# Kernel optimization log

Measured on AMD Instinct MI355X. Metric: run time of the kernel, lower is better.

Reference implementation:

```python
import jax, jax.numpy as jnp
import numpy as np

N = 8192      # nodes
E = 16384     # edges
G = 512       # graphs
IN = 235      # node feature dim (input_dim)
H = 64        # hidden_dim
ED = 52       # edge feature dim


def setup_inputs() -> dict:
    key = jax.random.key(0)
    ks = jax.random.split(key, 24)
    s = lambda fan_in: 1.0 / np.sqrt(fan_in)
    inp = {}
    inp["x"] = jax.random.normal(ks[0], (N, IN), dtype=jnp.float32)
    inp["edge_index"] = jax.random.randint(ks[1], (2, E), 0, N)
    inp["edge_attr"] = jax.random.uniform(ks[2], (E, ED), dtype=jnp.float32)
    inp["batch"] = jnp.sort(jax.random.randint(ks[3], (N,), 0, G))
    # EdgeModel (nn of nnconv1): Linear(52,128) -> Linear(128, 235*64)
    inp["W1"] = jax.random.normal(ks[4], (128, ED), dtype=jnp.float32) * s(ED)
    inp["b1"] = jnp.zeros((128,), jnp.float32)
    inp["W2"] = jax.random.normal(ks[5], (IN * H, 128), dtype=jnp.float32) * s(128)
    inp["b2"] = jnp.zeros((IN * H,), jnp.float32)
    # NNConv root weight and bias
    inp["root"] = jax.random.normal(ks[6], (IN, H), dtype=jnp.float32) * s(IN)
    inp["conv_b"] = jnp.zeros((H,), jnp.float32)
    # MLP head
    inp["fw1"] = jax.random.normal(ks[7], (128, H), dtype=jnp.float32) * s(H)
    inp["fb1"] = jnp.zeros((128,), jnp.float32)
    inp["fw2"] = jax.random.normal(ks[8], (256, 128), dtype=jnp.float32) * s(128)
    inp["fb2"] = jnp.zeros((256,), jnp.float32)
    inp["fw3"] = jax.random.normal(ks[9], (128, 256), dtype=jnp.float32) * s(256)
    inp["fb3"] = jnp.zeros((128,), jnp.float32)
    inp["fw4"] = jax.random.normal(ks[10], (1, 128), dtype=jnp.float32) * s(128)
    inp["fb4"] = jnp.zeros((1,), jnp.float32)
    return inp


def reference(x, edge_index, edge_attr, batch, W1, b1, W2, b2, root, conv_b,
              fw1, fb1, fw2, fb2, fw3, fb3, fw4, fb4):
    src, dst = edge_index[0], edge_index[1]
    # edge MLP -> per-edge weight matrices [E, IN, H]
    h = edge_attr @ W1.T + b1
    w = (h @ W2.T + b2).reshape(E, IN, H)
    # gather source node feats, per-edge matmul, scatter-add to destinations
    msg = jnp.einsum('ei,eih->eh', x[src], w)          # [E, H]
    agg = jax.ops.segment_sum(msg, dst, num_segments=N)  # [N, H]
    out = jax.nn.relu(agg + x @ root + conv_b)           # NNConv + ReLU
    # global mean pool per graph
    summ = jax.ops.segment_sum(out, batch, num_segments=G)
    cnt = jax.ops.segment_sum(jnp.ones((N, 1), out.dtype), batch, num_segments=G)
    pooled = summ / jnp.maximum(cnt, 1.0)                # [G, H]
    # dense MLP head
    y = jax.nn.relu(pooled @ fw1.T + fb1)
    y = jax.nn.relu(y @ fw2.T + fb2)
    y = jax.nn.relu(y @ fw3.T + fb3)
    return y @ fw4.T + fb4                               # [G, 1]
```

## Files before the change

### kernel.cpp

```cpp
#include <hip/hip_runtime.h>
#include <hip/hip_bf16.h>
#include <stdint.h>

#define N_NODES 8192
#define N_EDGES 16384
#define N_GRAPHS 512
#define IN_DIM 235
#define H_DIM 64
#define ED_DIM 52
#define HID1 128
#define KP 256
#define NB 3328
#define NBE 3456
#define NBP 3584

typedef __bf16 bf16x8 __attribute__((ext_vector_type(8)));
typedef float f32x4 __attribute__((ext_vector_type(4)));

static __device__ inline unsigned short f2bf(float f) {
    union { float f; unsigned u; } v; v.f = f;
    unsigned r = v.u + 0x7FFFu + ((v.u >> 16) & 1u);
    return (unsigned short)(r >> 16);
}

__global__ __launch_bounds__(256) void k_build_bt(const float* __restrict__ W1,
                                                  const float* __restrict__ W2,
                                                  unsigned short* __restrict__ Bt) {
    __shared__ float w1s[ED_DIM * 132];
    __shared__ float w2s[16 * 132];
    const int i = blockIdx.x;
    const int by = blockIdx.y;
    const int t = threadIdx.x;
    for (int j = t; j < ED_DIM * HID1; j += 256) {
        const int k = j / ED_DIM, d = j - k * ED_DIM;
        w1s[d * 132 + k] = W1[j];
    }
    const float* w2src = W2 + ((size_t)i * 64 + by * 16) * HID1;
    for (int j = t; j < 16 * HID1; j += 256) w2s[(j >> 7) * 132 + (j & 127)] = w2src[j];
    __syncthreads();
    const int hh = t & 15, dq = t >> 4;
    const float4* w2v = (const float4*)&w2s[hh * 132];
    #pragma unroll
    for (int m = 0; m < 4; ++m) {
        const int d = dq + m * 16;
        if (d >= ED_DIM) break;
        const float4* w1v = (const float4*)&w1s[d * 132];
        float acc = 0.f;
        #pragma unroll
        for (int k4 = 0; k4 < HID1 / 4; ++k4) {
            const float4 a = w1v[k4], b = w2v[k4];
            acc += a.x * b.x + a.y * b.y + a.z * b.z + a.w * b.w;
        }
        const int p = (by * 16 + hh) * ED_DIM + d;
        Bt[(size_t)p * KP + i] = f2bf(acc);
    }
}

__global__ __launch_bounds__(256) void k_build_ext(const float* __restrict__ root,
                                                   const float* __restrict__ W2,
                                                   const float* __restrict__ b1,
                                                   const float* __restrict__ b2,
                                                   unsigned short* __restrict__ Bt) {
    const int j = blockIdx.x;
    const int i = threadIdx.x;
    if (i >= IN_DIM) return;
    float v;
    if (j < 64) {
        v = root[i * H_DIM + j];
    } else {
        const int jj = i * H_DIM + (j - 64);
        float acc = b2[jj];
        const float* w = W2 + (size_t)jj * HID1;
        #pragma unroll 8
        for (int k = 0; k < HID1; ++k) acc += w[k] * b1[k];
        v = acc;
    }
    Bt[(size_t)(NB + j) * KP + i] = f2bf(v);
}

__global__ __launch_bounds__(256) void k_build_a(const float* __restrict__ x,
                                                 unsigned short* __restrict__ A) {
    const int j = blockIdx.x * 256 + threadIdx.x;
    const int n = j >> 8, i = j & 255;
    A[j] = (i < IN_DIM) ? f2bf(x[n * IN_DIM + i]) : (unsigned short)0;
}

__global__ __launch_bounds__(512, 2) void k_gemm(const unsigned short* __restrict__ A,
                                                 const unsigned short* __restrict__ Bt,
                                                 unsigned short* __restrict__ P,
                                                 float* __restrict__ agg,
                                                 float* __restrict__ xb2,
                                                 const float* __restrict__ conv_b) {
    __shared__ unsigned short As[2 * 256 * 32];
    __shared__ unsigned short Bs[2 * 256 * 32];
    const int t = threadIdx.x;
    const int lin = blockIdx.x;
    const int xcd = lin & 7, bi = lin >> 3;
    const int mt = (bi / 14) * 8 + xcd;
    const int nt = bi % 14;
    const int m0 = mt * 256, n0 = nt * 256;
    const int wid = t >> 6, lane = t & 63;
    const int wm = wid & 1;
    const int wn = wid >> 1;
    const int q = lane >> 4, r16 = lane & 15;

    f32x4 acc[8][4] = {};

    auto stage = [&](int k0, int buf) {
        #pragma unroll
        for (int r = 0; r < 2; ++r) {
            const int idx = r * 512 + t;
            const int row = idx >> 2;
            const int lgrp = ((idx & 3) ^ ((row >> 1) & 3)) * 8;
            const unsigned short* ga = &A[(size_t)(m0 + row) * KP + k0 + lgrp];
            const unsigned short* gb = &Bt[(size_t)(n0 + row) * KP + k0 + lgrp];
            char* la = (char*)As + buf * 16384 + r * 8192 + wid * 1024;
            char* lb = (char*)Bs + buf * 16384 + r * 8192 + wid * 1024;
            __builtin_amdgcn_global_load_lds(
                (const __attribute__((address_space(1))) unsigned int*)ga,
                (__attribute__((address_space(3))) unsigned int*)la, 16, 0, 0);
            __builtin_amdgcn_global_load_lds(
                (const __attribute__((address_space(1))) unsigned int*)gb,
                (__attribute__((address_space(3))) unsigned int*)lb, 16, 0, 0);
        }
    };

    stage(0, 0);
    const int pcq = (q ^ ((r16 >> 1) & 3)) * 8;
    #pragma unroll
    for (int it = 0; it < 8; ++it) {
        __syncthreads();
        if (it < 7) stage((it + 1) * 32, (it + 1) & 1);
        const int bo = (it & 1) * 8192;
        bf16x8 af[8], bfr[4];
        #pragma unroll
        for (int mi = 0; mi < 8; ++mi)
            af[mi] = *(const bf16x8*)(&As[bo + (wm * 128 + mi * 16 + r16) * 32 + pcq]);
        #pragma unroll
        for (int ni = 0; ni < 4; ++ni)
            bfr[ni] = *(const bf16x8*)(&Bs[bo + (wn * 64 + ni * 16 + r16) * 32 + pcq]);
        #pragma unroll
        for (int mi = 0; mi < 8; ++mi)
            #pragma unroll
            for (int ni = 0; ni < 4; ++ni)
                acc[mi][ni] = __builtin_amdgcn_mfma_f32_16x16x32_bf16(
                    bfr[ni], af[mi], acc[mi][ni], 0, 0, 0);
    }

    if (n0 < NB) {
        #pragma unroll
        for (int mi = 0; mi < 8; ++mi)
            #pragma unroll
            for (int ni = 0; ni < 4; ++ni) {
                const int row = m0 + wm * 128 + mi * 16 + r16;
                const int col = n0 + wn * 64 + ni * 16 + q * 4;
                union { unsigned short us[4]; uint2 u2; } pk;
                #pragma unroll
                for (int rr = 0; rr < 4; ++rr) pk.us[rr] = f2bf(acc[mi][ni][rr]);
                *(uint2*)(&P[(size_t)row * NB + col]) = pk.u2;
            }
    } else if (wn < 2) {
        #pragma unroll
        for (int mi = 0; mi < 8; ++mi)
            #pragma unroll
            for (int ni = 0; ni < 4; ++ni) {
                const int row = m0 + wm * 128 + mi * 16 + r16;
                const int cl = ni * 16 + q * 4;
                if (wn == 0) {
                    const float4 cb = *(const float4*)&conv_b[cl];
                    float4 v;
                    v.x = acc[mi][ni][0] + cb.x; v.y = acc[mi][ni][1] + cb.y;
                    v.z = acc[mi][ni][2] + cb.z; v.w = acc[mi][ni][3] + cb.w;
                    *(float4*)(&agg[row * H_DIM + cl]) = v;
                } else {
                    float4 v;
                    v.x = acc[mi][ni][0]; v.y = acc[mi][ni][1];
                    v.z = acc[mi][ni][2]; v.w = acc[mi][ni][3];
                    *(float4*)(&xb2[row * H_DIM + cl]) = v;
                }
            }
    }
}

__global__ __launch_bounds__(256) void k_edge(const int* __restrict__ ei,
                                              const float* __restrict__ ea,
                                              const unsigned short* __restrict__ P,
                                              const float* __restrict__ xb2,
                                              float* __restrict__ agg) {
    const int e = (blockIdx.x * 256 + threadIdx.x) >> 6;
    const int h = threadIdx.x & 63;
    if (e >= N_EDGES) return;
    const int s = ei[e], dst = ei[N_EDGES + e];
    const uint2* Pr = (const uint2*)(P + (size_t)s * NB + h * ED_DIM);
    const float4* ev = (const float4*)(ea + (size_t)e * ED_DIM);

    uint2 pv[13];
    #pragma unroll
    for (int j = 0; j < 13; ++j) pv[j] = Pr[j];
    float4 eav[13];
    #pragma unroll
    for (int j = 0; j < 13; ++j) eav[j] = ev[j];

    float acc = xb2[s * H_DIM + h];
    #pragma unroll
    for (int j = 0; j < 13; ++j) {
        union { unsigned u; float f; } a0, a1, b0, b1;
        a0.u = pv[j].x << 16; a1.u = pv[j].x & 0xffff0000u;
        b0.u = pv[j].y << 16; b1.u = pv[j].y & 0xffff0000u;
        acc += eav[j].x * a0.f + eav[j].y * a1.f
             + eav[j].z * b0.f + eav[j].w * b1.f;
    }
    atomicAdd(&agg[dst * H_DIM + h], acc);
}

__global__ __launch_bounds__(256) void k_pool(const float* __restrict__ agg,
                                              const int* __restrict__ batch,
                                              float* __restrict__ psum,
                                              float* __restrict__ pcnt) {
    const int n = (blockIdx.x * 256 + threadIdx.x) >> 6;
    const int h = threadIdx.x & 63;
    if (n >= N_NODES) return;
    const float v = fmaxf(agg[n * H_DIM + h], 0.f);
    const int g = batch[n];
    atomicAdd(&psum[g * H_DIM + h], v);
    if (h == 0) atomicAdd(&pcnt[g], 1.0f);
}

__global__ __launch_bounds__(256) void k_head(const float* __restrict__ psum,
                                              const float* __restrict__ pcnt,
                                              const float* __restrict__ fw1, const float* __restrict__ fb1,
                                              const float* __restrict__ fw2, const float* __restrict__ fb2,
                                              const float* __restrict__ fw3, const float* __restrict__ fb3,
                                              const float* __restrict__ fw4, const float* __restrict__ fb4,
                                              float* __restrict__ out) {
    __shared__ float sp[64], s1[128], s2[256], s3[128];
    const int g = blockIdx.x, t = threadIdx.x;
    if (t < 64) sp[t] = psum[g * 64 + t] / fmaxf(pcnt[g], 1.0f);
    __syncthreads();
    if (t < 128) {
        float a = fb1[t];
        const float* w = fw1 + t * 64;
        #pragma unroll 8
        for (int k = 0; k < 64; ++k) a += sp[k] * w[k];
        s1[t] = fmaxf(a, 0.f);
    }
    __syncthreads();
    {
        float a = fb2[t];
        const float* w = fw2 + t * 128;
        #pragma unroll 8
        for (int k = 0; k < 128; ++k) a += s1[k] * w[k];
        s2[t] = fmaxf(a, 0.f);
    }
    __syncthreads();
    if (t < 128) {
        float a = fb3[t];
        const float* w = fw3 + t * 256;
        #pragma unroll 8
        for (int k = 0; k < 256; ++k) a += s2[k] * w[k];
        s3[t] = fmaxf(a, 0.f);
    }
    __syncthreads();
    if (t < 64) {
        float p = s3[t] * fw4[t] + s3[t + 64] * fw4[t + 64];
        #pragma unroll
        for (int off = 32; off > 0; off >>= 1) p += __shfl_down(p, off);
        if (t == 0) out[g] = p + fb4[0];
    }
}

extern "C" void kernel_launch(void* const* d_in, const int* in_sizes, int n_in,
                              void* d_out, int out_size, void* d_ws, size_t ws_size,
                              hipStream_t stream) {
    const float* x      = (const float*)d_in[0];
    const int*   ei     = (const int*)d_in[1];
    const float* ea     = (const float*)d_in[2];
    const int*   batch  = (const int*)d_in[3];
    const float* W1     = (const float*)d_in[4];
    const float* b1     = (const float*)d_in[5];
    const float* W2     = (const float*)d_in[6];
    const float* b2     = (const float*)d_in[7];
    const float* root   = (const float*)d_in[8];
    const float* conv_b = (const float*)d_in[9];
    const float* fw1 = (const float*)d_in[10]; const float* fb1 = (const float*)d_in[11];
    const float* fw2 = (const float*)d_in[12]; const float* fb2 = (const float*)d_in[13];
    const float* fw3 = (const float*)d_in[14]; const float* fb3 = (const float*)d_in[15];
    const float* fw4 = (const float*)d_in[16]; const float* fb4 = (const float*)d_in[17];
    float* out = (float*)d_out;

    char* ws = (char*)d_ws;
    unsigned short* A   = (unsigned short*)(ws);
    unsigned short* Bt  = (unsigned short*)(ws + 4194304);
    unsigned short* P   = (unsigned short*)(ws + 6029312);
    float* agg  = (float*)(ws + 60555264);
    float* xb2  = (float*)(ws + 62652416);
    float* psum = (float*)(ws + 64749568);
    float* pcnt = (float*)(ws + 64880640);

    hipMemsetAsync(Bt, 0, (size_t)NBP * KP * sizeof(unsigned short), stream);
    hipMemsetAsync(psum, 0, (size_t)(N_GRAPHS * H_DIM + N_GRAPHS) * sizeof(float), stream);

    k_build_bt<<<dim3(IN_DIM, 4), dim3(256), 0, stream>>>(W1, W2, Bt);
    k_build_ext<<<dim3(128), dim3(256), 0, stream>>>(root, W2, b1, b2, Bt);
    k_build_a<<<dim3(N_NODES), dim3(256), 0, stream>>>(x, A);
    k_gemm<<<dim3(448), dim3(512), 0, stream>>>(A, Bt, P, agg, xb2, conv_b);
    k_edge<<<dim3(N_EDGES / 4), dim3(256), 0, stream>>>(ei, ea, P, xb2, agg);
    k_pool<<<dim3(N_NODES / 4), dim3(256), 0, stream>>>(agg, batch, psum, pcnt);
    k_head<<<dim3(N_GRAPHS), dim3(256), 0, stream>>>(psum, pcnt, fw1, fb1, fw2, fb2, fw3, fb3, fw4, fb4, out);
}
```

Measured before the change: 208.1 us.

## Fuse prep kernels, replace Bt memset with targeted zeroing, fuse pool into head

The three weight and input preparation kernels are merged into one launch. The full Bt memset is replaced by blocks that zero only the padding regions. The atomic-based pooling kernel and its memset are removed: each head block binary-searches the sorted batch array for its node range and reduces that range in shared memory before running the MLP. This cuts four launches and two memsets and removes the pooling atomics. The cost is some uneven block work in the fused prep kernel and a reliance on batch being sorted.

```diff
diff --git a/kernel.cpp b/kernel.cpp
--- a/kernel.cpp
+++ b/kernel.cpp
@@ -11,8 +11,12 @@
 #define HID1 128
 #define KP 256
 #define NB 3328
-#define NBE 3456
 #define NBP 3584
+
+#define BT_BLOCKS 940
+#define EXT_BLOCKS 128
+#define ZERO_BLOCKS 16
+#define PREP_GRID (BT_BLOCKS + EXT_BLOCKS + ZERO_BLOCKS + N_NODES)
 
 typedef __bf16 bf16x8 __attribute__((ext_vector_type(8)));
 typedef float f32x4 __attribute__((ext_vector_type(4)));
@@ -23,66 +27,83 @@
     return (unsigned short)(r >> 16);
 }
 
-__global__ __launch_bounds__(256) void k_build_bt(const float* __restrict__ W1,
-                                                  const float* __restrict__ W2,
-                                                  unsigned short* __restrict__ Bt) {
+__global__ __launch_bounds__(256) void k_prep(const float* __restrict__ x,
+                                              const float* __restrict__ W1,
+                                              const float* __restrict__ W2,
+                                              const float* __restrict__ b1,
+                                              const float* __restrict__ b2,
+                                              const float* __restrict__ root,
+                                              unsigned short* __restrict__ A,
+                                              unsigned short* __restrict__ Bt) {
     __shared__ float w1s[ED_DIM * 132];
     __shared__ float w2s[16 * 132];
-    const int i = blockIdx.x;
-    const int by = blockIdx.y;
+    const int bx = blockIdx.x;
     const int t = threadIdx.x;
-    for (int j = t; j < ED_DIM * HID1; j += 256) {
-        const int k = j / ED_DIM, d = j - k * ED_DIM;
-        w1s[d * 132 + k] = W1[j];
-    }
-    const float* w2src = W2 + ((size_t)i * 64 + by * 16) * HID1;
-    for (int j = t; j < 16 * HID1; j += 256) w2s[(j >> 7) * 132 + (j & 127)] = w2src[j];
-    __syncthreads();
-    const int hh = t & 15, dq = t >> 4;
-    const float4* w2v = (const float4*)&w2s[hh * 132];
-    #pragma unroll
-    for (int m = 0; m < 4; ++m) {
-        const int d = dq + m * 16;
-        if (d >= ED_DIM) break;
-        const float4* w1v = (const float4*)&w1s[d * 132];
-        float acc = 0.f;
-        #pragma unroll
-        for (int k4 = 0; k4 < HID1 / 4; ++k4) {
-            const float4 a = w1v[k4], b = w2v[k4];
-            acc += a.x * b.x + a.y * b.y + a.z * b.z + a.w * b.w;
-        }
-        const int p = (by * 16 + hh) * ED_DIM + d;
-        Bt[(size_t)p * KP + i] = f2bf(acc);
-    }
-}
-
-__global__ __launch_bounds__(256) void k_build_ext(const float* __restrict__ root,
-                                                   const float* __restrict__ W2,
-                                                   const float* __restrict__ b1,
-                                                   const float* __restrict__ b2,
-                                                   unsigned short* __restrict__ Bt) {
-    const int j = blockIdx.x;
-    const int i = threadIdx.x;
-    if (i >= IN_DIM) return;
-    float v;
-    if (j < 64) {
-        v = root[i * H_DIM + j];
+
+    if (bx < BT_BLOCKS) {
+        const int i = bx >> 2;
+        const int by = bx & 3;
+        for (int j = t; j < ED_DIM * HID1; j += 256) {
+            const int k = j / ED_DIM, d = j - k * ED_DIM;
+            w1s[d * 132 + k] = W1[j];
+        }
+        const float* w2src = W2 + ((size_t)i * 64 + by * 16) * HID1;
+        for (int j = t; j < 16 * HID1; j += 256) w2s[(j >> 7) * 132 + (j & 127)] = w2src[j];
+        __syncthreads();
+        const int hh = t & 15, dq = t >> 4;
+        const float4* w2v = (const float4*)&w2s[hh * 132];
+        #pragma unroll
+        for (int m = 0; m < 4; ++m) {
+            const int d = dq + m * 16;
+            if (d >= ED_DIM) break;
+            const float4* w1v = (const float4*)&w1s[d * 132];
+            float acc = 0.f;
+            #pragma unroll
+            for (int k4 = 0; k4 < HID1 / 4; ++k4) {
+                const float4 a = w1v[k4], b = w2v[k4];
+                acc += a.x * b.x + a.y * b.y + a.z * b.z + a.w * b.w;
+            }
+            const int p = (by * 16 + hh) * ED_DIM + d;
+            Bt[(size_t)p * KP + i] = f2bf(acc);
+        }
+    } else if (bx < BT_BLOCKS + EXT_BLOCKS) {
+        const int j = bx - BT_BLOCKS;
+        const int i = t;
+        if (i < IN_DIM) {
+            float v;
+            if (j < 64) {
+                v = root[i * H_DIM + j];
+            } else {
+                const int jj = i * H_DIM + (j - 64);
+                float acc = b2[jj];
+                const float* w = W2 + (size_t)jj * HID1;
+                #pragma unroll 8
+                for (int k = 0; k < HID1; ++k) acc += w[k] * b1[k];
+                v = acc;
+            }
+            Bt[(size_t)(NB + j) * KP + i] = f2bf(v);
+        }
+    } else if (bx < BT_BLOCKS + EXT_BLOCKS + ZERO_BLOCKS) {
+        const int z = bx - BT_BLOCKS - EXT_BLOCKS;
+        const int R1 = NBP * 21;
+        const int TOT = R1 + 128 * IN_DIM;
+        for (int idx = z * 256 + t; idx < TOT; idx += ZERO_BLOCKS * 256) {
+            size_t off;
+            if (idx < R1) {
+                const int r = idx / 21, c = IN_DIM + idx - (idx / 21) * 21;
+                off = (size_t)r * KP + c;
+            } else {
+                const int k = idx - R1;
+                const int r = 3456 + k / IN_DIM, c = k - (k / IN_DIM) * IN_DIM;
+                off = (size_t)r * KP + c;
+            }
+            Bt[off] = 0;
+        }
     } else {
-        const int jj = i * H_DIM + (j - 64);
-        float acc = b2[jj];
-        const float* w = W2 + (size_t)jj * HID1;
-        #pragma unroll 8
-        for (int k = 0; k < HID1; ++k) acc += w[k] * b1[k];
-        v = acc;
-    }
-    Bt[(size_t)(NB + j) * KP + i] = f2bf(v);
-}
-
-__global__ __launch_bounds__(256) void k_build_a(const float* __restrict__ x,
-                                                 unsigned short* __restrict__ A) {
-    const int j = blockIdx.x * 256 + threadIdx.x;
-    const int n = j >> 8, i = j & 255;
-    A[j] = (i < IN_DIM) ? f2bf(x[n * IN_DIM + i]) : (unsigned short)0;
+        const int j = (bx - BT_BLOCKS - EXT_BLOCKS - ZERO_BLOCKS) * 256 + t;
+        const int n = j >> 8, i = j & 255;
+        A[j] = (i < IN_DIM) ? f2bf(x[n * IN_DIM + i]) : (unsigned short)0;
+    }
 }
 
 __global__ __launch_bounds__(512, 2) void k_gemm(const unsigned short* __restrict__ A,
@@ -213,52 +234,55 @@
     atomicAdd(&agg[dst * H_DIM + h], acc);
 }
 
-__global__ __launch_bounds__(256) void k_pool(const float* __restrict__ agg,
+__global__ __launch_bounds__(256) void k_tail(const float* __restrict__ agg,
                                               const int* __restrict__ batch,
-                                              float* __restrict__ psum,
-                                              float* __restrict__ pcnt) {
-    const int n = (blockIdx.x * 256 + threadIdx.x) >> 6;
-    const int h = threadIdx.x & 63;
-    if (n >= N_NODES) return;
-    const float v = fmaxf(agg[n * H_DIM + h], 0.f);
-    const int g = batch[n];
-    atomicAdd(&psum[g * H_DIM + h], v);
-    if (h == 0) atomicAdd(&pcnt[g], 1.0f);
-}
-
-__global__ __launch_bounds__(256) void k_head(const float* __restrict__ psum,
-                                              const float* __restrict__ pcnt,
                                               const float* __restrict__ fw1, const float* __restrict__ fb1,
                                               const float* __restrict__ fw2, const float* __restrict__ fb2,
                                               const float* __restrict__ fw3, const float* __restrict__ fb3,
                                               const float* __restrict__ fw4, const float* __restrict__ fb4,
                                               float* __restrict__ out) {
+    __shared__ float red[256];
     __shared__ float sp[64], s1[128], s2[256], s3[128];
     const int g = blockIdx.x, t = threadIdx.x;
-    if (t < 64) sp[t] = psum[g * 64 + t] / fmaxf(pcnt[g], 1.0f);
-    __syncthreads();
+
+    int lo = 0, hi = N_NODES;
+    while (lo < hi) { const int mid = (lo + hi) >> 1; if (batch[mid] < g) lo = mid + 1; else hi = mid; }
+    const int start = lo;
+    hi = N_NODES;
+    while (lo < hi) { const int mid = (lo + hi) >> 1; if (batch[mid] <= g) lo = mid + 1; else hi = mid; }
+    const int end = lo;
+    const float inv = 1.0f / fmaxf((float)(end - start), 1.0f);
+
+    float a = 0.f;
+    for (int n = start + (t >> 6); n < end; n += 4)
+        a += fmaxf(agg[n * H_DIM + (t & 63)], 0.f);
+    red[t] = a;
+    __syncthreads();
+    if (t < 64) sp[t] = (red[t] + red[t + 64] + red[t + 128] + red[t + 192]) * inv;
+    __syncthreads();
+
     if (t < 128) {
-        float a = fb1[t];
+        float acc = fb1[t];
         const float* w = fw1 + t * 64;
         #pragma unroll 8
-        for (int k = 0; k < 64; ++k) a += sp[k] * w[k];
-        s1[t] = fmaxf(a, 0.f);
+        for (int k = 0; k < 64; ++k) acc += sp[k] * w[k];
+        s1[t] = fmaxf(acc, 0.f);
     }
     __syncthreads();
     {
-        float a = fb2[t];
+        float acc = fb2[t];
         const float* w = fw2 + t * 128;
         #pragma unroll 8
-        for (int k = 0; k < 128; ++k) a += s1[k] * w[k];
-        s2[t] = fmaxf(a, 0.f);
+        for (int k = 0; k < 128; ++k) acc += s1[k] * w[k];
+        s2[t] = fmaxf(acc, 0.f);
     }
     __syncthreads();
     if (t < 128) {
-        float a = fb3[t];
+        float acc = fb3[t];
         const float* w = fw3 + t * 256;
         #pragma unroll 8
-        for (int k = 0; k < 256; ++k) a += s2[k] * w[k];
-        s3[t] = fmaxf(a, 0.f);
+        for (int k = 0; k < 256; ++k) acc += s2[k] * w[k];
+        s3[t] = fmaxf(acc, 0.f);
     }
     __syncthreads();
     if (t < 64) {
@@ -294,17 +318,9 @@
     unsigned short* P   = (unsigned short*)(ws + 6029312);
     float* agg  = (float*)(ws + 60555264);
     float* xb2  = (float*)(ws + 62652416);
-    float* psum = (float*)(ws + 64749568);
-    float* pcnt = (float*)(ws + 64880640);
-
-    hipMemsetAsync(Bt, 0, (size_t)NBP * KP * sizeof(unsigned short), stream);
-    hipMemsetAsync(psum, 0, (size_t)(N_GRAPHS * H_DIM + N_GRAPHS) * sizeof(float), stream);
-
-    k_build_bt<<<dim3(IN_DIM, 4), dim3(256), 0, stream>>>(W1, W2, Bt);
-    k_build_ext<<<dim3(128), dim3(256), 0, stream>>>(root, W2, b1, b2, Bt);
-    k_build_a<<<dim3(N_NODES), dim3(256), 0, stream>>>(x, A);
+
+    k_prep<<<dim3(PREP_GRID), dim3(256), 0, stream>>>(x, W1, W2, b1, b2, root, A, Bt);
     k_gemm<<<dim3(448), dim3(512), 0, stream>>>(A, Bt, P, agg, xb2, conv_b);
     k_edge<<<dim3(N_EDGES / 4), dim3(256), 0, stream>>>(ei, ea, P, xb2, agg);
-    k_pool<<<dim3(N_NODES / 4), dim3(256), 0, stream>>>(agg, batch, psum, pcnt);
-    k_head<<<dim3(N_GRAPHS), dim3(256), 0, stream>>>(psum, pcnt, fw1, fb1, fw2, fb2, fw3, fb3, fw4, fb4, out);
-}
+    k_tail<<<dim3(N_GRAPHS), dim3(256), 0, stream>>>(agg, batch, fw1, fb1, fw2, fb2, fw3, fb3, fw4, fb4, out);
+}
```

New measurement: 189.2 us. 9.1% less time.
